# Performance work log

Measured on AMD Instinct MI355X. Metric: run time of the kernel, lower is better.

Reference implementation:

```python
import jax, jax.numpy as jnp
import numpy as np

D_MODEL = 2048
NUM_HEADS = 16
D_K = D_MODEL // NUM_HEADS
SEQ = 2048
BATCH = 2
THETA = 10000.0


def setup_inputs() -> dict:
    key = jax.random.key(0)
    ks = jax.random.split(key, 5)
    s = 1.0 / np.sqrt(D_MODEL)
    return {
        "x": jax.random.normal(ks[0], (BATCH, SEQ, D_MODEL), jnp.float32),
        "wq": jax.random.normal(ks[1], (D_MODEL, D_MODEL), jnp.float32) * s,
        "wk": jax.random.normal(ks[2], (D_MODEL, D_MODEL), jnp.float32) * s,
        "wv": jax.random.normal(ks[3], (D_MODEL, D_MODEL), jnp.float32) * s,
        "wo": jax.random.normal(ks[4], (D_MODEL, D_MODEL), jnp.float32) * s,
    }


def _rope_tables(seq_len, d_k, theta, dtype):
    pos = jnp.arange(seq_len, dtype=dtype)[:, None]            # [S,1]
    inv = theta ** (-(jnp.arange(0, d_k, 2, dtype=dtype) / d_k))  # [d_k/2]
    ang = pos * inv                                            # [S, d_k/2]
    sin = jnp.repeat(jnp.sin(ang), 2, axis=1)                  # [S, d_k] interleaved
    cos = jnp.repeat(jnp.cos(ang), 2, axis=1)
    return sin, cos


def _apply_rope(x, sin, cos):
    # x: [..., S, d_k]; interleaved-pair rotation
    xp = x.reshape(x.shape[:-1] + (x.shape[-1] // 2, 2))
    swapped = jnp.stack((-xp[..., 1], xp[..., 0]), axis=-1).reshape(x.shape)
    return x * cos + swapped * sin


def reference(x, wq, wk, wv, wo):
    B, S, D = x.shape
    H, dk = NUM_HEADS, D_K
    # projections: weights are (H*dk, D); q/k/v -> [B,H,S,dk]
    q = jnp.einsum("bsd,hkd->bhsk", x, wq.reshape(H, dk, D))
    k = jnp.einsum("bsd,hkd->bhsk", x, wk.reshape(H, dk, D))
    v = jnp.einsum("bsd,hkd->bhsk", x, wv.reshape(H, dk, D))
    sin, cos = _rope_tables(S, dk, THETA, x.dtype)
    q = _apply_rope(q, sin, cos)
    k = _apply_rope(k, sin, cos)
    scores = jnp.einsum("bhqk,bhsk->bhqs", q, k) / jnp.sqrt(jnp.asarray(dk, x.dtype))
    causal = jnp.triu(jnp.ones((S, S), dtype=bool), k=1)
    scores = jnp.where(causal, -jnp.inf, scores)
    attn = jax.nn.softmax(scores, axis=-1)
    out = jnp.einsum("bhqs,bhsv->bqhv", attn, v).reshape(B, S, H * dk)
    return jnp.einsum("bsf,df->bsd", out, wo)
```

## Files before the change

kernel.cpp:

```cpp
#include <hip/hip_runtime.h>
#include <hip/hip_bf16.h>

#define B_  2
#define S_  2048
#define D_  2048
#define H_  16
#define DK_ 128
#define M_  (B_*S_)

typedef unsigned short u16;
typedef short bf16x8 __attribute__((ext_vector_type(8)));
typedef float f32x4  __attribute__((ext_vector_type(4)));

#define NEG_BIG (-1.0e30f)

__device__ __forceinline__ u16 f2bf(float f){
    unsigned int u = __float_as_uint(f);
    unsigned int r = (u + 0x7fffu + ((u >> 16) & 1u)) >> 16;
    return (u16)r;
}

__device__ __forceinline__ uint4 cvt8(const float* p){
    float4 a = *(const float4*)p;
    float4 b = *(const float4*)(p + 4);
    uint4 r;
    r.x = ((unsigned int)f2bf(a.y) << 16) | (unsigned int)f2bf(a.x);
    r.y = ((unsigned int)f2bf(a.w) << 16) | (unsigned int)f2bf(a.z);
    r.z = ((unsigned int)f2bf(b.y) << 16) | (unsigned int)f2bf(b.x);
    r.w = ((unsigned int)f2bf(b.w) << 16) | (unsigned int)f2bf(b.z);
    return r;
}

__device__ __forceinline__ void unpack8(const uint4 v, float* f){
    f[0]=__uint_as_float(v.x<<16); f[1]=__uint_as_float(v.x&0xffff0000u);
    f[2]=__uint_as_float(v.y<<16); f[3]=__uint_as_float(v.y&0xffff0000u);
    f[4]=__uint_as_float(v.z<<16); f[5]=__uint_as_float(v.z&0xffff0000u);
    f[6]=__uint_as_float(v.w<<16); f[7]=__uint_as_float(v.w&0xffff0000u);
}

__device__ __forceinline__ void async16(const void* g, void* l){
    __builtin_amdgcn_global_load_lds(
        (const __attribute__((address_space(1))) void*)g,
        (__attribute__((address_space(3))) void*)l, 16, 0, 0);
}

__global__ __launch_bounds__(256) void cvt_all(
    const float* __restrict__ x,  const float* __restrict__ wq, const float* __restrict__ wk,
    const float* __restrict__ wv, const float* __restrict__ wo,
    u16* __restrict__ xb, u16* __restrict__ wqb, u16* __restrict__ wkb,
    u16* __restrict__ wvb, u16* __restrict__ wob)
{
    int c = blockIdx.x*256 + threadIdx.x;
    const float* src; u16* dst; int lc;
    if      (c < 1048576){ src = x;  dst = xb;  lc = c; }
    else if (c < 1572864){ src = wq; dst = wqb; lc = c - 1048576; }
    else if (c < 2097152){ src = wk; dst = wkb; lc = c - 1572864; }
    else if (c < 2621440){ src = wv; dst = wvb; lc = c - 2097152; }
    else                 { src = wo; dst = wob; lc = c - 2621440; }
    *(uint4*)&dst[(size_t)lc*8] = cvt8(&src[(size_t)lc*8]);
}

__global__ __launch_bounds__(512, 2) void gemm4ph(
    const u16* __restrict__ A, const u16* __restrict__ W0, const u16* __restrict__ W1,
    u16* __restrict__ C0, u16* __restrict__ C1)
{
    __shared__ __align__(16) u16 Ab[2][256*64];
    __shared__ __align__(16) u16 Bb[2][256*64];

    const int tid  = threadIdx.x;
    const int lane = tid & 63;
    const int w    = tid >> 6;
    const int quad = lane >> 4;
    const int l15  = lane & 15;
    const int wM   = w & 1;
    const int wN   = w >> 1;
    const int bH   = w >> 2;
    const int cw   = w >> 1;
    const int cb   = w & 3;
    const int sw   = l15 & 7;
    const int blockN = blockIdx.x * 256;
    const int blockM = blockIdx.y * 256;

    const u16* Wm = blockIdx.z ? W1 : W0;
    u16*       Cm = blockIdx.z ? C1 : C0;

    f32x4 acc[32];
    #pragma unroll
    for (int i = 0; i < 32; ++i) acc[i] = (f32x4){0.f,0.f,0.f,0.f};

    auto stageA = [&](int t, int l){
        int c  = l*256 + cw*64 + lane;
        int ra = c >> 3, g = c & 7;
        int cl = g ^ (ra & 7);
        int kb = t*64 + cl*8;
        async16(&A[(size_t)(blockM + wM*128 + ra)*2048 + kb],
                &Ab[t & 1][wM*8192 + c*8]);
    };
    auto stageB = [&](int t, int l){
        int c  = l*256 + cb*64 + lane;
        int rb = c >> 3, g = c & 7;
        int cl = g ^ (rb & 7);
        int kb = t*64 + cl*8;
        async16(&Wm[(size_t)(blockN + bH*128 + rb)*2048 + kb],
                &Bb[t & 1][bH*8192 + c*8]);
    };

    stageB(0,0); stageB(0,1); stageB(0,2); stageB(0,3);
    stageA(0,0); stageA(0,1); stageA(0,2); stageA(0,3);
    asm volatile("s_waitcnt vmcnt(2)" ::: "memory");
    __builtin_amdgcn_s_barrier();
    __builtin_amdgcn_sched_barrier(0);

    for (int t = 0; t < 32; ++t){
        const u16* ab = &Ab[t & 1][0];
        const u16* bb = &Bb[t & 1][0];
        const bool st = (t < 31);
        bf16x8 bfv[4][2], af[2][2];

        #pragma unroll
        for (int ni = 0; ni < 4; ++ni)
            #pragma unroll
            for (int kk = 0; kk < 2; ++kk)
                bfv[ni][kk] = *(const bf16x8*)&bb[(wN*64 + ni*16 + l15)*64 + (((kk*4+quad) ^ sw))*8];
        #pragma unroll
        for (int j = 0; j < 2; ++j)
            #pragma unroll
            for (int kk = 0; kk < 2; ++kk)
                af[j][kk] = *(const bf16x8*)&ab[(wM*128 + (0+j)*16 + l15)*64 + (((kk*4+quad) ^ sw))*8];
        if (st){ stageB(t+1, 0); stageB(t+1, 1); }
        __builtin_amdgcn_s_barrier();
        asm volatile("s_waitcnt lgkmcnt(0)" ::: "memory");
        __builtin_amdgcn_sched_barrier(0);
        __builtin_amdgcn_s_setprio(1);
        #pragma unroll
        for (int j = 0; j < 2; ++j)
            #pragma unroll
            for (int ni = 0; ni < 4; ++ni)
                #pragma unroll
                for (int kk = 0; kk < 2; ++kk)
                    acc[(0+j)*4 + ni] = __builtin_amdgcn_mfma_f32_16x16x32_bf16(
                        af[j][kk], bfv[ni][kk], acc[(0+j)*4 + ni], 0, 0, 0);
        __builtin_amdgcn_s_setprio(0);
        __builtin_amdgcn_s_barrier();
        __builtin_amdgcn_sched_barrier(0);

        #pragma unroll
        for (int j = 0; j < 2; ++j)
            #pragma unroll
            for (int kk = 0; kk < 2; ++kk)
                af[j][kk] = *(const bf16x8*)&ab[(wM*128 + (2+j)*16 + l15)*64 + (((kk*4+quad) ^ sw))*8];
        if (st){ stageB(t+1, 2); stageB(t+1, 3); }
        __builtin_amdgcn_s_barrier();
        asm volatile("s_waitcnt lgkmcnt(0)" ::: "memory");
        __builtin_amdgcn_sched_barrier(0);
        __builtin_amdgcn_s_setprio(1);
        #pragma unroll
        for (int j = 0; j < 2; ++j)
            #pragma unroll
            for (int ni = 0; ni < 4; ++ni)
                #pragma unroll
                for (int kk = 0; kk < 2; ++kk)
                    acc[(2+j)*4 + ni] = __builtin_amdgcn_mfma_f32_16x16x32_bf16(
                        af[j][kk], bfv[ni][kk], acc[(2+j)*4 + ni], 0, 0, 0);
        __builtin_amdgcn_s_setprio(0);
        if (st) { asm volatile("s_waitcnt vmcnt(4)" ::: "memory"); }
        else    { asm volatile("s_waitcnt vmcnt(0)" ::: "memory"); }
        __builtin_amdgcn_s_barrier();
        __builtin_amdgcn_sched_barrier(0);

        #pragma unroll
        for (int j = 0; j < 2; ++j)
            #pragma unroll
            for (int kk = 0; kk < 2; ++kk)
                af[j][kk] = *(const bf16x8*)&ab[(wM*128 + (4+j)*16 + l15)*64 + (((kk*4+quad) ^ sw))*8];
        if (st){ stageA(t+1, 0); stageA(t+1, 1); }
        __builtin_amdgcn_s_barrier();
        asm volatile("s_waitcnt lgkmcnt(0)" ::: "memory");
        __builtin_amdgcn_sched_barrier(0);
        __builtin_amdgcn_s_setprio(1);
        #pragma unroll
        for (int j = 0; j < 2; ++j)
            #pragma unroll
            for (int ni = 0; ni < 4; ++ni)
                #pragma unroll
                for (int kk = 0; kk < 2; ++kk)
                    acc[(4+j)*4 + ni] = __builtin_amdgcn_mfma_f32_16x16x32_bf16(
                        af[j][kk], bfv[ni][kk], acc[(4+j)*4 + ni], 0, 0, 0);
        __builtin_amdgcn_s_setprio(0);
        __builtin_amdgcn_s_barrier();
        __builtin_amdgcn_sched_barrier(0);

        #pragma unroll
        for (int j = 0; j < 2; ++j)
            #pragma unroll
            for (int kk = 0; kk < 2; ++kk)
                af[j][kk] = *(const bf16x8*)&ab[(wM*128 + (6+j)*16 + l15)*64 + (((kk*4+quad) ^ sw))*8];
        if (st){ stageA(t+1, 2); stageA(t+1, 3); }
        __builtin_amdgcn_s_barrier();
        asm volatile("s_waitcnt lgkmcnt(0)" ::: "memory");
        __builtin_amdgcn_sched_barrier(0);
        __builtin_amdgcn_s_setprio(1);
        #pragma unroll
        for (int j = 0; j < 2; ++j)
            #pragma unroll
            for (int ni = 0; ni < 4; ++ni)
                #pragma unroll
                for (int kk = 0; kk < 2; ++kk)
                    acc[(6+j)*4 + ni] = __builtin_amdgcn_mfma_f32_16x16x32_bf16(
                        af[j][kk], bfv[ni][kk], acc[(6+j)*4 + ni], 0, 0, 0);
        __builtin_amdgcn_s_setprio(0);
        if (st) { asm volatile("s_waitcnt vmcnt(2)" ::: "memory"); }
        __builtin_amdgcn_s_barrier();
        __builtin_amdgcn_sched_barrier(0);
    }

    #pragma unroll
    for (int mi = 0; mi < 8; ++mi){
        #pragma unroll
        for (int ni = 0; ni < 4; ++ni){
            #pragma unroll
            for (int r = 0; r < 4; ++r){
                float v = acc[mi*4 + ni][r];
                int row = blockM + wM*128 + mi*16 + quad*4 + r;
                int col = blockN + wN*64 + ni*16 + l15;
                int b = row >> 11, s2 = row & 2047;
                int h = col >> 7,  kk = col & 127;
                Cm[(((size_t)(b*H_ + h))*S_ + s2)*DK_ + kk] = f2bf(v);
            }
        }
    }
}

template<int MODE, int NF>
__global__ __launch_bounds__(512, 2) void gemm256(
    const u16* __restrict__ A, const u16* __restrict__ W0, const u16* __restrict__ W1,
    void* __restrict__ C0, void* __restrict__ C1)
{
    constexpr int BN = NF * 64;
    __shared__ __align__(16) u16 ring[4][(256 + BN) * 32];

    const int tid  = threadIdx.x;
    const int lane = tid & 63;
    const int w    = tid >> 6;
    const int quad = lane >> 4;
    const int l15  = lane & 15;
    const int wM   = w & 1;
    const int wN   = w >> 1;
    const int blockN = blockIdx.x * BN;
    const int blockM = blockIdx.y * 256;

    const u16* Wm; void* Cm;
    if (MODE == 0){ Wm = blockIdx.z ? W1 : W0; Cm = blockIdx.z ? (void*)C1 : (void*)C0; }
    else          { Wm = W0; Cm = C0; }

    const int cswz = quad ^ ((l15 >> 1) & 3);

    f32x4 acc[8 * NF];
    #pragma unroll
    for (int i = 0; i < 8 * NF; ++i) acc[i] = (f32x4){0.f,0.f,0.f,0.f};

    auto stage = [&](int t){
        const int k0 = t * 32;
        u16* la = (u16*)&ring[t & 3][0];
        u16* lb = la + 256*32;
        #pragma unroll
        for (int it = 0; it < 2; ++it){
            int cc  = it*512 + tid;
            int row = cc >> 2;
            int g   = (cc & 3) ^ ((cc >> 3) & 3);
            int kb  = k0 + g*8;
            const u16* ga;
            if (MODE == 1){
                int rg = blockM + row;
                int b = rg >> 11, s2 = rg & 2047;
                int h = kb >> 7,  kk = kb & 127;
                ga = &A[(((size_t)(b*H_ + h))*S_ + s2)*DK_ + kk];
            } else {
                ga = &A[(size_t)(blockM + row)*2048 + kb];
            }
            async16(ga, la + cc*8);
        }
        #pragma unroll
        for (int it = 0; it < BN/128; ++it){
            int cc  = it*512 + tid;
            int row = cc >> 2;
            int g   = (cc & 3) ^ ((cc >> 3) & 3);
            int kb  = k0 + g*8;
            async16(&Wm[(size_t)(blockN + row)*2048 + kb], lb + cc*8);
        }
    };

    stage(0); stage(1); stage(2);
    if constexpr (NF == 4) asm volatile("s_waitcnt vmcnt(8)" ::: "memory");
    else                   asm volatile("s_waitcnt vmcnt(6)" ::: "memory");
    __builtin_amdgcn_s_barrier();
    __builtin_amdgcn_sched_barrier(0);

    for (int t = 0; t < 64; ++t){
        const u16* la = (const u16*)&ring[t & 3][0];
        const u16* lb = la + 256*32;

        if (t <= 60) stage(t + 3);

        bf16x8 bfv[NF];
        #pragma unroll
        for (int ni = 0; ni < NF; ++ni)
            bfv[ni] = *(const bf16x8*)&lb[(wN*(NF*16) + ni*16 + l15)*32 + cswz*8];

        #pragma unroll
        for (int hf = 0; hf < 2; ++hf){
            bf16x8 af[4];
            #pragma unroll
            for (int mi = 0; mi < 4; ++mi)
                af[mi] = *(const bf16x8*)&la[(wM*128 + hf*64 + mi*16 + l15)*32 + cswz*8];
            __builtin_amdgcn_s_setprio(1);
            #pragma unroll
            for (int mi = 0; mi < 4; ++mi)
                #pragma unroll
                for (int ni = 0; ni < NF; ++ni)
                    acc[(hf*4 + mi)*NF + ni] = __builtin_amdgcn_mfma_f32_16x16x32_bf16(
                        af[mi], bfv[ni], acc[(hf*4 + mi)*NF + ni], 0, 0, 0);
            __builtin_amdgcn_s_setprio(0);
        }

        if constexpr (NF == 4){
            if (t <= 60)      { asm volatile("s_waitcnt vmcnt(8)" ::: "memory"); }
            else if (t == 61) { asm volatile("s_waitcnt vmcnt(4)" ::: "memory"); }
            else if (t == 62) { asm volatile("s_waitcnt vmcnt(0)" ::: "memory"); }
        } else {
            if (t <= 60)      { asm volatile("s_waitcnt vmcnt(6)" ::: "memory"); }
            else if (t == 61) { asm volatile("s_waitcnt vmcnt(3)" ::: "memory"); }
            else if (t == 62) { asm volatile("s_waitcnt vmcnt(0)" ::: "memory"); }
        }
        __builtin_amdgcn_s_barrier();
        __builtin_amdgcn_sched_barrier(0);
    }

    #pragma unroll
    for (int hf = 0; hf < 2; ++hf){
        #pragma unroll
        for (int mi = 0; mi < 4; ++mi){
            #pragma unroll
            for (int ni = 0; ni < NF; ++ni){
                #pragma unroll
                for (int r = 0; r < 4; ++r){
                    float v = acc[(hf*4 + mi)*NF + ni][r];
                    int row = blockM + wM*128 + hf*64 + mi*16 + quad*4 + r;
                    int col = blockN + wN*(NF*16) + ni*16 + l15;
                    if (MODE == 0){
                        int b = row >> 11, s2 = row & 2047;
                        int h = col >> 7,  kk = col & 127;
                        ((u16*)Cm)[(((size_t)(b*H_ + h))*S_ + s2)*DK_ + kk] = f2bf(v);
                    } else if (MODE == 2){
                        int h = row >> 7,  kk = row & 127;
                        int b = col >> 11, s2 = col & 2047;
                        ((u16*)Cm)[(((size_t)(b*H_ + h))*DK_ + kk)*S_ + s2] = f2bf(v);
                    } else {
                        ((float*)Cm)[(size_t)row*2048 + col] = v;
                    }
                }
            }
        }
    }
}

template<int MODE>
__global__ __launch_bounds__(256) void gemm_bt(
    const void* __restrict__ Av,
    const float* __restrict__ W0, const float* __restrict__ W1,
    void* __restrict__ C0, void* __restrict__ C1)
{
    __shared__ u16 As[128*40];
    __shared__ u16 Bs[128*40];

    const int tid  = threadIdx.x;
    const int lane = tid & 63;
    const int w    = tid >> 6;
    const int quad = lane >> 4;
    const int l15  = lane & 15;
    const int blockN = blockIdx.x * 128;
    const int blockM = blockIdx.y * 128;

    const float* Wm; void* Cm;
    if (MODE == 0){ Wm = blockIdx.z ? W1 : W0; Cm = blockIdx.z ? (void*)C1 : (void*)C0; }
    else          { Wm = W0; Cm = C0; }

    const int waveM = (w & 1) * 64;
    const int waveN = (w >> 1) * 64;

    f32x4 acc[16];
    #pragma unroll
    for (int i = 0; i < 16; ++i) acc[i] = (f32x4){0.f,0.f,0.f,0.f};

    for (int k0 = 0; k0 < 2048; k0 += 32){
        __syncthreads();
        #pragma unroll
        for (int it = 0; it < 2; ++it){
            int cc  = tid + it*256;
            int row = cc >> 2;
            int ch  = cc & 3;
            int kb  = k0 + ch*8;
            uint4 va;
            if (MODE == 1){
                int g = blockM + row;
                int b = g >> 11, s2 = g & 2047;
                int h = kb >> 7, kk = kb & 127;
                va = *(const uint4*)&((const u16*)Av)[(((size_t)(b*H_ + h))*S_ + s2)*DK_ + kk];
            } else {
                va = cvt8(&((const float*)Av)[(size_t)(blockM+row)*2048 + kb]);
            }
            uint4 vb = cvt8(&Wm[(size_t)(blockN+row)*2048 + kb]);
            *(uint4*)&As[row*40 + ch*8] = va;
            *(uint4*)&Bs[row*40 + ch*8] = vb;
        }
        __syncthreads();

        bf16x8 af[4], bfv[4];
        #pragma unroll
        for (int mi = 0; mi < 4; ++mi)
            af[mi]  = *(const bf16x8*)&As[(waveM + mi*16 + l15)*40 + quad*8];
        #pragma unroll
        for (int ni = 0; ni < 4; ++ni)
            bfv[ni] = *(const bf16x8*)&Bs[(waveN + ni*16 + l15)*40 + quad*8];
        #pragma unroll
        for (int mi = 0; mi < 4; ++mi)
            #pragma unroll
            for (int ni = 0; ni < 4; ++ni)
                acc[mi*4+ni] = __builtin_amdgcn_mfma_f32_16x16x32_bf16(
                                   af[mi], bfv[ni], acc[mi*4+ni], 0, 0, 0);
    }

    #pragma unroll
    for (int mi = 0; mi < 4; ++mi){
        #pragma unroll
        for (int ni = 0; ni < 4; ++ni){
            #pragma unroll
            for (int r = 0; r < 4; ++r){
                float v = acc[mi*4+ni][r];
                int row = blockM + waveM + mi*16 + quad*4 + r;
                int col = blockN + waveN + ni*16 + l15;
                if (MODE == 0){
                    int b = row >> 11, s2 = row & 2047;
                    int h = col >> 7,  kk = col & 127;
                    ((u16*)Cm)[(((size_t)(b*H_ + h))*S_ + s2)*DK_ + kk] = f2bf(v);
                } else if (MODE == 2){
                    int h = row >> 7,  kk = row & 127;
                    int b = col >> 11, s2 = col & 2047;
                    ((u16*)Cm)[(((size_t)(b*H_ + h))*DK_ + kk)*S_ + s2] = f2bf(v);
                } else {
                    ((float*)Cm)[(size_t)row*2048 + col] = v;
                }
            }
        }
    }
}

__global__ __launch_bounds__(256) void rope_kernel(u16* __restrict__ Q, u16* __restrict__ K)
{
    u16* T = blockIdx.y ? K : Q;
    const float osc = blockIdx.y ? 1.0f : 0.12751743f;
    int t  = blockIdx.x * 256 + threadIdx.x;
    int i0 = (t & 15) * 4;
    int s  = (t >> 4) & 2047;
    size_t base = ((size_t)(t >> 4)) * 128 + (size_t)i0 * 2;
    uint4 v = *(const uint4*)&T[base];
    float f[8]; unpack8(v, f);
    const float nl2t = -13.287712379549449f / 64.0f;
    float sf = (float)s;
    unsigned int out[4];
    #pragma unroll
    for (int p = 0; p < 4; ++p){
        float inv = exp2f((float)(i0 + p) * nl2t);
        float ang = sf * inv;
        float sn, cn;
        sincosf(ang, &sn, &cn);
        float e0 = f[2*p], e1 = f[2*p+1];
        float r0 = (e0*cn - e1*sn) * osc;
        float r1 = (e1*cn + e0*sn) * osc;
        out[p] = ((unsigned int)f2bf(r1) << 16) | (unsigned int)f2bf(r0);
    }
    uint4 ov; ov.x = out[0]; ov.y = out[1]; ov.z = out[2]; ov.w = out[3];
    *(uint4*)&T[base] = ov;
}

__global__ __launch_bounds__(256, 4) void attn_mfma(
    const u16* Q, const u16* __restrict__ K,
    const u16* __restrict__ VT, u16* O)
{
    __shared__ __align__(16) u16 Ks[2][64*128];
    __shared__ __align__(16) u16 Vs[2][128*64];
    __shared__ __align__(16) u16 Ps[4][16*64];

    const int tid  = threadIdx.x;
    const int bh   = blockIdx.x;
    const int qb   = (int)gridDim.y - 1 - (int)blockIdx.y;
    const int w    = tid >> 6;
    const int lane = tid & 63;
    const int quad = lane >> 4;
    const int l15  = lane & 15;
    const int sw   = l15 & 7;
    const size_t qkb = (size_t)bh * S_ * DK_;

    const int qw = qb*64 + w*16;

    bf16x8 aq[4];
    {
        const u16* qp = &Q[qkb + (size_t)(qw + l15)*128 + quad*8];
        #pragma unroll
        for (int kt = 0; kt < 4; ++kt)
            aq[kt] = *(const bf16x8*)(qp + kt*32);
    }

    f32x4 oa[8];
    #pragma unroll
    for (int vt = 0; vt < 8; ++vt) oa[vt] = (f32x4){0.f,0.f,0.f,0.f};
    float l_i = 0.f;

    auto stage = [&](int kb, int buf){
        #pragma unroll
        for (int it = 0; it < 4; ++it){
            int cc  = tid + it*256;
            int row = cc >> 4, cl = cc & 15;
            async16(&K[qkb + (size_t)(kb*64 + row)*128 + (size_t)((cl ^ (row & 7))*8)],
                    &Ks[buf][cc*8]);
        }
        #pragma unroll
        for (int it = 0; it < 4; ++it){
            int cc  = tid + it*256;
            int row = cc >> 3, cl = cc & 7;
            async16(&VT[qkb + (size_t)row*S_ + (size_t)(kb*64 + (cl ^ (row & 7))*8)],
                    &Vs[buf][cc*8]);
        }
    };

    const int nkb = qb + 1;
    stage(0, 0);
    __syncthreads();

    for (int kb = 0; kb < nkb; ++kb){
        const int cur = kb & 1;
        if (kb + 1 < nkb) stage(kb + 1, cur ^ 1);

        const u16* ks = &Ks[cur][0];
        const u16* vs = &Vs[cur][0];

        f32x4 s[4];
        __builtin_amdgcn_s_setprio(1);
        #pragma unroll
        for (int nt = 0; nt < 4; ++nt){
            f32x4 a = (f32x4){0.f,0.f,0.f,0.f};
            #pragma unroll
            for (int kt = 0; kt < 4; ++kt){
                bf16x8 ak = *(const bf16x8*)&ks[(nt*16 + l15)*128 + ((kt*4 + quad) ^ sw)*8];
                a = __builtin_amdgcn_mfma_f32_16x16x32_bf16(ak, aq[kt], a, 0,0,0);
            }
            s[nt] = a;
        }
        __builtin_amdgcn_s_setprio(0);

        if (kb == nkb - 1){
            int qg = qw + l15;
            #pragma unroll
            for (int nt = 0; nt < 4; ++nt)
                #pragma unroll
                for (int rr = 0; rr < 4; ++rr){
                    int jg = kb*64 + nt*16 + quad*4 + rr;
                    if (jg > qg) s[nt][rr] = NEG_BIG;
                }
        }

        float ps = 0.f;
        #pragma unroll
        for (int nt = 0; nt < 4; ++nt)
            #pragma unroll
            for (int rr = 0; rr < 4; ++rr){
                float p = exp2f(s[nt][rr] - 16.0f);
                s[nt][rr] = p; ps += p;
            }
        ps += __shfl_xor(ps, 16, 64);
        ps += __shfl_xor(ps, 32, 64);
        l_i += ps;

        u16* pw = Ps[w];
        #pragma unroll
        for (int nt = 0; nt < 4; ++nt){
            uint2 pk;
            asm("v_cvt_pk_bf16_f32 %0, %1, %2" : "=v"(pk.x) : "v"(s[nt][0]), "v"(s[nt][1]));
            asm("v_cvt_pk_bf16_f32 %0, %1, %2" : "=v"(pk.y) : "v"(s[nt][2]), "v"(s[nt][3]));
            int c = (nt*2 + (quad >> 1)) ^ sw;
            *(uint2*)&pw[l15*64 + c*8 + (quad & 1)*4] = pk;
        }

        bf16x8 pa[2];
        #pragma unroll
        for (int kt = 0; kt < 2; ++kt)
            pa[kt] = *(const bf16x8*)&pw[l15*64 + ((kt*4 + quad) ^ sw)*8];

        __builtin_amdgcn_s_setprio(1);
        #pragma unroll
        for (int vt = 0; vt < 8; ++vt){
            #pragma unroll
            for (int kt = 0; kt < 2; ++kt){
                bf16x8 bv = *(const bf16x8*)&vs[(vt*16 + l15)*64 + ((kt*4 + quad) ^ sw)*8];
                oa[vt] = __builtin_amdgcn_mfma_f32_16x16x32_bf16(pa[kt], bv, oa[vt], 0,0,0);
            }
        }
        __builtin_amdgcn_s_setprio(0);

        __syncthreads();
    }

    #pragma unroll
    for (int rr = 0; rr < 4; ++rr){
        float lv = __shfl(l_i, (lane & 48) | (quad*4 + rr), 64);
        float inv = 1.f / lv;
        int qg = qw + quad*4 + rr;
        #pragma unroll
        for (int vt = 0; vt < 8; ++vt)
            O[qkb + (size_t)qg*128 + vt*16 + l15] = f2bf(oa[vt][rr] * inv);
    }
}

extern "C" void kernel_launch(void* const* d_in, const int* in_sizes, int n_in,
                              void* d_out, int out_size, void* d_ws, size_t ws_size,
                              hipStream_t stream)
{
    const float* x  = (const float*)d_in[0];
    const float* wq = (const float*)d_in[1];
    const float* wk = (const float*)d_in[2];
    const float* wv = (const float*)d_in[3];
    const float* wo = (const float*)d_in[4];
    float* out = (float*)d_out;

    const size_t NT = (size_t)B_ * H_ * S_ * DK_;
    const size_t NW = (size_t)D_ * D_;

    if (ws_size >= (size_t)50331648){
        u16* Qw  = (u16*)d_ws;
        u16* Kw  = Qw + NT;
        u16* wvb = Qw + 2*NT;
        u16* wob = wvb + NW;
        u16* xb  = (u16*)d_out;
        u16* wqb = xb + NT;
        u16* wkb = wqb + NW;
        u16* VT  = xb + NT;
        u16* Ow  = Qw;

        cvt_all<<<dim3(12288), 256, 0, stream>>>(x, wq, wk, wv, wo,
                                                 xb, wqb, wkb, wvb, wob);
        gemm4ph<<<dim3(8, 16, 2), 512, 0, stream>>>(xb, wqb, wkb, Qw, Kw);
        gemm256<2,2><<<dim3(32, 8, 1), 512, 0, stream>>>(wvb, xb, nullptr, VT, nullptr);
        rope_kernel<<<dim3(4096, 2), 256, 0, stream>>>(Qw, Kw);
        attn_mfma<<<dim3(32, 32), 256, 0, stream>>>(Qw, Kw, VT, Ow);
        gemm256<1,2><<<dim3(16, 16, 1), 512, 0, stream>>>(Ow, wob, nullptr, out, nullptr);
    } else {
        u16* Qw  = (u16*)d_ws;
        u16* Vtd = (u16*)d_out;
        u16* Kw  = (u16*)d_out + NT;
        u16* Ow  = Qw;
        gemm_bt<0><<<dim3(16, 32, 2), 256, 0, stream>>>(x, wq, wk, Qw, Kw);
        gemm_bt<2><<<dim3(32, 16, 1), 256, 0, stream>>>(wv, x, nullptr, Vtd, nullptr);
        rope_kernel<<<dim3(4096, 2), 256, 0, stream>>>(Qw, Kw);
        attn_mfma<<<dim3(32, 32), 256, 0, stream>>>(Qw, Kw, Vtd, Ow);
        gemm_bt<1><<<dim3(16, 32, 1), 256, 0, stream>>>(Ow, wo, nullptr, out, nullptr);
    }
}
```

Before: 358.7 us.

## Fuse RoPE into QK projection epilogue and load V directly from global

Applies the RoPE rotation and the Q scale inside the gemm4ph epilogue, using a lane shuffle to fetch the pair partner, and drops the separate rope_kernel launch on the large-workspace path. The attention kernel stops staging V tiles in shared memory. Each lane instead loads its V fragments straight from global memory into registers, and launch bounds drop to 3 blocks per CU. This removes one full read and write pass over Q and K plus the V LDS traffic, but it adds sincos work to the GEMM epilogue, uncoalesced, unpipelined global V loads and higher register pressure. The fast __sincosf may also lose accuracy at large angles.

```diff
diff --git a/kernel.cpp b/kernel.cpp
--- a/kernel.cpp
+++ b/kernel.cpp
@@ -214,6 +214,8 @@
         __builtin_amdgcn_sched_barrier(0);
     }
 
+    const float osc  = blockIdx.z ? 1.0f : 0.12751743f;
+    const float nl2t = -13.287712379549449f / 64.0f;
     #pragma unroll
     for (int mi = 0; mi < 8; ++mi){
         #pragma unroll
@@ -223,9 +225,15 @@
                 float v = acc[mi*4 + ni][r];
                 int row = blockM + wM*128 + mi*16 + quad*4 + r;
                 int col = blockN + wN*64 + ni*16 + l15;
+                float pv = __shfl_xor(v, 1, 64);
+                int ii = (col >> 1) & 63;
+                float inv = exp2f((float)ii * nl2t);
+                float ang = (float)(row & 2047) * inv;
+                float sn, cn; __sincosf(ang, &sn, &cn);
+                float rv = ((col & 1) ? (v*cn + pv*sn) : (v*cn - pv*sn)) * osc;
                 int b = row >> 11, s2 = row & 2047;
                 int h = col >> 7,  kk = col & 127;
-                Cm[(((size_t)(b*H_ + h))*S_ + s2)*DK_ + kk] = f2bf(v);
+                Cm[(((size_t)(b*H_ + h))*S_ + s2)*DK_ + kk] = f2bf(rv);
             }
         }
     }
@@ -483,12 +491,11 @@
     *(uint4*)&T[base] = ov;
 }
 
-__global__ __launch_bounds__(256, 4) void attn_mfma(
+__global__ __launch_bounds__(256, 3) void attn_mfma(
     const u16* Q, const u16* __restrict__ K,
     const u16* __restrict__ VT, u16* O)
 {
     __shared__ __align__(16) u16 Ks[2][64*128];
-    __shared__ __align__(16) u16 Vs[2][128*64];
     __shared__ __align__(16) u16 Ps[4][16*64];
 
     const int tid  = threadIdx.x;
@@ -516,7 +523,7 @@
     for (int vt = 0; vt < 8; ++vt) oa[vt] = (f32x4){0.f,0.f,0.f,0.f};
     float l_i = 0.f;
 
-    auto stage = [&](int kb, int buf){
+    auto stageK = [&](int kb, int buf){
         #pragma unroll
         for (int it = 0; it < 4; ++it){
             int cc  = tid + it*256;
@@ -524,25 +531,19 @@
             async16(&K[qkb + (size_t)(kb*64 + row)*128 + (size_t)((cl ^ (row & 7))*8)],
                     &Ks[buf][cc*8]);
         }
-        #pragma unroll
-        for (int it = 0; it < 4; ++it){
-            int cc  = tid + it*256;
-            int row = cc >> 3, cl = cc & 7;
-            async16(&VT[qkb + (size_t)row*S_ + (size_t)(kb*64 + (cl ^ (row & 7))*8)],
-                    &Vs[buf][cc*8]);
-        }
     };
 
     const int nkb = qb + 1;
-    stage(0, 0);
+    stageK(0, 0);
     __syncthreads();
+
+    const u16* vbase = VT + qkb + (size_t)l15*2048 + quad*8;
 
     for (int kb = 0; kb < nkb; ++kb){
         const int cur = kb & 1;
-        if (kb + 1 < nkb) stage(kb + 1, cur ^ 1);
+        if (kb + 1 < nkb) stageK(kb + 1, cur ^ 1);
 
         const u16* ks = &Ks[cur][0];
-        const u16* vs = &Vs[cur][0];
 
         f32x4 s[4];
         __builtin_amdgcn_s_setprio(1);
@@ -557,6 +558,16 @@
             s[nt] = a;
         }
         __builtin_amdgcn_s_setprio(0);
+
+        bf16x8 bv[8][2];
+        {
+            const u16* vb = vbase + kb*64;
+            #pragma unroll
+            for (int vt = 0; vt < 8; ++vt)
+                #pragma unroll
+                for (int kt = 0; kt < 2; ++kt)
+                    bv[vt][kt] = *(const bf16x8*)(vb + (size_t)vt*16*2048 + kt*32);
+        }
 
         if (kb == nkb - 1){
             int qg = qw + l15;
@@ -598,13 +609,10 @@
 
         __builtin_amdgcn_s_setprio(1);
         #pragma unroll
-        for (int vt = 0; vt < 8; ++vt){
-            #pragma unroll
-            for (int kt = 0; kt < 2; ++kt){
-                bf16x8 bv = *(const bf16x8*)&vs[(vt*16 + l15)*64 + ((kt*4 + quad) ^ sw)*8];
-                oa[vt] = __builtin_amdgcn_mfma_f32_16x16x32_bf16(pa[kt], bv, oa[vt], 0,0,0);
-            }
-        }
+        for (int vt = 0; vt < 8; ++vt)
+            #pragma unroll
+            for (int kt = 0; kt < 2; ++kt)
+                oa[vt] = __builtin_amdgcn_mfma_f32_16x16x32_bf16(pa[kt], bv[vt][kt], oa[vt], 0,0,0);
         __builtin_amdgcn_s_setprio(0);
 
         __syncthreads();
@@ -650,7 +658,6 @@
                                                  xb, wqb, wkb, wvb, wob);
         gemm4ph<<<dim3(8, 16, 2), 512, 0, stream>>>(xb, wqb, wkb, Qw, Kw);
         gemm256<2,2><<<dim3(32, 8, 1), 512, 0, stream>>>(wvb, xb, nullptr, VT, nullptr);
-        rope_kernel<<<dim3(4096, 2), 256, 0, stream>>>(Qw, Kw);
         attn_mfma<<<dim3(32, 32), 256, 0, stream>>>(Qw, Kw, VT, Ow);
         gemm256<1,2><<<dim3(16, 16, 1), 512, 0, stream>>>(Ow, wob, nullptr, out, nullptr);
     } else {
```

Measured after the change: 420.3 us. +17.2%, slower.
